# Optimization experiments

Measured on AMD Instinct MI355X. Metric: run time of the kernel, lower is better.

The kernel has to match this reference:

```python
import jax, jax.numpy as jnp
import numpy as np

NUM_HEADS = 12

def setup_inputs() -> dict:
    key = jax.random.key(0)
    k1, k2, k3, k4 = jax.random.split(key, 4)
    B, N, D = 8, 1024, 768
    x = jax.random.normal(k1, (B, N, D), dtype=jnp.float32)
    mask = jax.random.randint(k2, (B, N), 0, 2, dtype=jnp.int32)
    Wqkv = jax.random.normal(k3, (3 * D, D), dtype=jnp.float32) * (D ** -0.5)
    Wproj = jax.random.normal(k4, (D, D), dtype=jnp.float32) * (D ** -0.5)
    bproj = jnp.zeros((D,), dtype=jnp.float32)
    return {"x": x, "mask": mask, "Wqkv": Wqkv, "Wproj": Wproj, "bproj": bproj}

def reference(x, mask, Wqkv, Wproj, bproj):
    B, N, D = x.shape
    H = NUM_HEADS
    hd = D // H
    scale = hd ** -0.5
    # QKV projection (no bias), split into q,k,v of shape [B,H,N,hd]
    qkv = jnp.einsum('bnd,ed->bne', x, Wqkv).reshape(B, N, 3, H, hd)
    qkv = jnp.transpose(qkv, (2, 0, 3, 1, 4))
    q, k, v = qkv[0], qkv[1], qkv[2]
    # padding mask: attend where both query and key are valid; masked-out
    # (padded) query rows attend only to themselves (diagonal) to avoid NaNs
    m = mask.astype(bool)  # [B,N]
    pair = m[:, None, :, None] & m[:, None, None, :]          # [B,1,N,N]
    diag = jnp.eye(N, dtype=bool)[None, None]                 # [1,1,N,N]
    attn_mask = pair | (diag & ~m[:, None, :, None])          # [B,1,N,N]
    scores = jnp.einsum('bhnd,bhmd->bhnm', q, k) * scale      # [B,H,N,N]
    scores = jnp.where(attn_mask, scores, jnp.finfo(scores.dtype).min)
    attn = jax.nn.softmax(scores, axis=-1)
    out = jnp.einsum('bhnm,bhmd->bhnd', attn, v)
    out = jnp.transpose(out, (0, 2, 1, 3)).reshape(B, N, D)
    out = jnp.einsum('bnd,ed->bne', out, Wproj) + bproj
    return out
```

## Files before the change

kernel.cpp:

```cpp
#include <hip/hip_runtime.h>
#include <hip/hip_bf16.h>
#include <stdint.h>


typedef unsigned short u16;
typedef __attribute__((ext_vector_type(8))) short short8;
typedef __attribute__((ext_vector_type(4))) float f32x4;

#define MFMA16(a, b, c) __builtin_amdgcn_mfma_f32_16x16x32_bf16((a), (b), (c), 0, 0, 0)

static __device__ __forceinline__ u16 f2bf(float f) {
    __hip_bfloat16 h = __float2bfloat16(f);
    return *(u16*)&h;
}
static __device__ __forceinline__ void gld16(const u16* g, u16* l) {
  __builtin_amdgcn_global_load_lds(
      (const __attribute__((address_space(1))) void*)g,
      (__attribute__((address_space(3))) void*)l, 16, 0, 0);
}

__global__ __launch_bounds__(256) void cvt_bf16(
    const float* __restrict__ s0, u16* __restrict__ d0, int n0,
    const float* __restrict__ s1, u16* __restrict__ d1, int n1,
    const float* __restrict__ s2, u16* __restrict__ d2, int n2) {
  int i = (blockIdx.x * 256 + threadIdx.x) * 4;
  const float* s; u16* d;
  if (i < n0) { s = s0 + i; d = d0 + i; }
  else if ((i -= n0) < n1) { s = s1 + i; d = d1 + i; }
  else if ((i -= n1) < n2) { s = s2 + i; d = d2 + i; }
  else return;
  float4 v = *(const float4*)s;
  ushort4 o;
  o.x = f2bf(v.x); o.y = f2bf(v.y); o.z = f2bf(v.z); o.w = f2bf(v.w);
  *(ushort4*)d = o;
}

template<int K, int BN, int LDC, bool BF16OUT>
__global__ __launch_bounds__(256) void gemm_bt(
    const u16* __restrict__ A,
    const u16* __restrict__ B,
    void* __restrict__ Cout,
    const float* __restrict__ bias) {
  constexpr int NT = BN / 32;
  __shared__ u16 As[128 * 32];
  __shared__ u16 Bs[BN * 32];
  const int tid = threadIdx.x;
  const int w = tid >> 6, l = tid & 63;
  const int lane16 = l & 15, quad = l >> 4;
  const int i0 = blockIdx.y * 128, j0 = blockIdx.x * BN;
  const int mh = (w & 1) * 64;
  const int nh = (w >> 1) * (BN / 2);

  f32x4 acc[4][NT];
  #pragma unroll
  for (int mt = 0; mt < 4; mt++)
    #pragma unroll
    for (int nt = 0; nt < NT; nt++) acc[mt][nt] = (f32x4){0.f, 0.f, 0.f, 0.f};

  for (int kt = 0; kt < K / 32; kt++) {
    const int k0 = kt * 32;
    __syncthreads();
    #pragma unroll
    for (int s = 0; s < 2; s++) {
      int idx = tid + s * 256;
      int row = idx >> 2, c8 = (idx & 3) * 8;
      gld16(&A[(size_t)(i0 + row) * K + k0 + c8], &As[idx * 8]);
    }
    #pragma unroll
    for (int s = 0; s < BN / 64; s++) {
      int idx = tid + s * 256;
      int row = idx >> 2, c8 = (idx & 3) * 8;
      gld16(&B[(size_t)(j0 + row) * K + k0 + c8], &Bs[idx * 8]);
    }
    __syncthreads();

    short8 af[4], bf[NT];
    #pragma unroll
    for (int mt = 0; mt < 4; mt++)
      af[mt] = *(const short8*)&As[(mh + mt * 16 + lane16) * 32 + quad * 8];
    #pragma unroll
    for (int nt = 0; nt < NT; nt++)
      bf[nt] = *(const short8*)&Bs[(nh + nt * 16 + lane16) * 32 + quad * 8];
    #pragma unroll
    for (int mt = 0; mt < 4; mt++)
      #pragma unroll
      for (int nt = 0; nt < NT; nt++)
        acc[mt][nt] = MFMA16(af[mt], bf[nt], acc[mt][nt]);
  }

  #pragma unroll
  for (int mt = 0; mt < 4; mt++) {
    #pragma unroll
    for (int nt = 0; nt < NT; nt++) {
      int col = j0 + nh + nt * 16 + lane16;
      #pragma unroll
      for (int r = 0; r < 4; r++) {
        int row = i0 + mh + mt * 16 + quad * 4 + r;
        if (BF16OUT) {
          ((u16*)Cout)[(size_t)row * LDC + col] = f2bf(acc[mt][nt][r]);
        } else {
          ((float*)Cout)[(size_t)row * LDC + col] = acc[mt][nt][r] + bias[col];
        }
      }
    }
  }
}

__global__ __launch_bounds__(256, 4) void attn_mfma(
    const u16* __restrict__ qkv,
    const int* __restrict__ mask,
    u16* __restrict__ ctx) {
  __shared__ u16 Ks[64][72];
  __shared__ u16 Vt[64][72];
  __shared__ u16 Ps[4][32][72];
  __shared__ float mkb[64];
  __shared__ int mqs[128];

  const int tid = threadIdx.x;
  const int w = tid >> 6, l = tid & 63;
  const int lane16 = l & 15, quad = l >> 4;
  const int idx = blockIdx.x;
  const int bh = idx % 96;
  const int rb = idx / 96;
  const int b = bh / 12, h = bh % 12;
  const int n0 = rb * 128;
  const int baseRow = b * 1024;

  const int key_s = tid >> 2, ds_s = (tid & 3) * 16;
  const int kA_s = (tid & 31) * 2, dg_s = tid >> 5;

  if (tid < 128) mqs[tid] = mask[baseRow + n0 + tid];

  short8 qfrag[2][2];
  #pragma unroll
  for (int qt = 0; qt < 2; qt++) {
    const u16* qp = qkv + (size_t)(baseRow + n0 + w*32 + qt*16 + lane16) * 2304 + h*64;
    #pragma unroll
    for (int ks = 0; ks < 2; ks++)
      qfrag[qt][ks] = *(const short8*)(qp + ks*32 + quad*8);
  }

  f32x4 oacc[2][4];
  #pragma unroll
  for (int qt = 0; qt < 2; qt++)
    #pragma unroll
    for (int nt = 0; nt < 4; nt++) oacc[qt][nt] = (f32x4){0.f, 0.f, 0.f, 0.f};
  float lsum[2] = {0.f, 0.f};

  const float K1 = 0.18033688011112043f;
  const float K0 = -23.083120654223415f;

  for (int c = 0; c < 16; c++) {
    if (c) __syncthreads();
    {
      const u16* kp = qkv + (size_t)(baseRow + c*64 + key_s) * 2304 + 768 + h*64 + ds_s;
      uint4 kr0 = *(const uint4*)kp;
      uint4 kr1 = *(const uint4*)(kp + 8);
      const u16* vp = qkv + (size_t)(baseRow + c*64 + kA_s) * 2304 + 1536 + h*64 + dg_s*8;
      uint4 vr0 = *(const uint4*)vp;
      uint4 vr1 = *(const uint4*)(vp + 2304);
      *(uint4*)&Ks[key_s][ds_s]     = kr0;
      *(uint4*)&Ks[key_s][ds_s + 8] = kr1;
      const u16* va = (const u16*)&vr0;
      const u16* vb = (const u16*)&vr1;
      #pragma unroll
      for (int j = 0; j < 8; j++)
        *(unsigned int*)&Vt[dg_s*8 + j][kA_s] =
            (unsigned int)va[j] | ((unsigned int)vb[j] << 16);
      if (tid < 64) mkb[tid] = mask[baseRow + c*64 + tid] ? 0.f : -1e38f;
    }
    __syncthreads();

    f32x4 sacc[4][2];
    #pragma unroll
    for (int kt = 0; kt < 4; kt++)
      #pragma unroll
      for (int qt = 0; qt < 2; qt++) sacc[kt][qt] = (f32x4){0.f, 0.f, 0.f, 0.f};
    #pragma unroll
    for (int ks = 0; ks < 2; ks++) {
      short8 kf[4];
      #pragma unroll
      for (int kt = 0; kt < 4; kt++)
        kf[kt] = *(const short8*)&Ks[kt*16 + lane16][ks*32 + quad*8];
      #pragma unroll
      for (int kt = 0; kt < 4; kt++)
        #pragma unroll
        for (int qt = 0; qt < 2; qt++)
          sacc[kt][qt] = MFMA16(kf[kt], qfrag[qt][ks], sacc[kt][qt]);
    }

    #pragma unroll
    for (int kt = 0; kt < 4; kt++) {
      #pragma unroll
      for (int qt = 0; qt < 2; qt++) {
        u16 pk[4];
        #pragma unroll
        for (int r = 0; r < 4; r++) {
          int keyl = kt*16 + quad*4 + r;
          float e = __builtin_amdgcn_exp2f(fmaf(sacc[kt][qt][r], K1, K0) + mkb[keyl]);
          lsum[qt] += e;
          pk[r] = f2bf(e);
        }
        uint2 pv;
        pv.x = (unsigned int)pk[0] | ((unsigned int)pk[1] << 16);
        pv.y = (unsigned int)pk[2] | ((unsigned int)pk[3] << 16);
        *(uint2*)&Ps[w][qt*16 + lane16][kt*16 + quad*4] = pv;
      }
    }

    #pragma unroll
    for (int kc = 0; kc < 2; kc++) {
      short8 pf[2], vf[4];
      #pragma unroll
      for (int qt = 0; qt < 2; qt++)
        pf[qt] = *(const short8*)&Ps[w][qt*16 + lane16][kc*32 + quad*8];
      #pragma unroll
      for (int nt = 0; nt < 4; nt++)
        vf[nt] = *(const short8*)&Vt[nt*16 + lane16][kc*32 + quad*8];
      #pragma unroll
      for (int qt = 0; qt < 2; qt++)
        #pragma unroll
        for (int nt = 0; nt < 4; nt++)
          oacc[qt][nt] = MFMA16(pf[qt], vf[nt], oacc[qt][nt]);
    }
  }

  float linv[2][4];
  #pragma unroll
  for (int qt = 0; qt < 2; qt++) {
    float s = lsum[qt];
    s += __shfl_xor(s, 16);
    s += __shfl_xor(s, 32);
    #pragma unroll
    for (int r = 0; r < 4; r++)
      linv[qt][r] = 1.0f / __shfl(s, quad*4 + r);
  }
  #pragma unroll
  for (int qt = 0; qt < 2; qt++) {
    #pragma unroll
    for (int r = 0; r < 4; r++) {
      int rl = w*32 + qt*16 + quad*4 + r;
      int rg = n0 + rl;
      int mq = mqs[rl];
      #pragma unroll
      for (int nt = 0; nt < 4; nt++) {
        u16 outv;
        if (mq) {
          outv = f2bf(oacc[qt][nt][r] * linv[qt][r]);
        } else {
          outv = qkv[(size_t)(baseRow + rg) * 2304 + 1536 + h*64 + nt*16 + lane16];
        }
        ctx[(size_t)(baseRow + rg) * 768 + h*64 + nt*16 + lane16] = outv;
      }
    }
  }
}

extern "C" void kernel_launch(void* const* d_in, const int* in_sizes, int n_in,
                              void* d_out, int out_size, void* d_ws, size_t ws_size,
                              hipStream_t stream) {
  const float* x     = (const float*)d_in[0];
  const int*   mask  = (const int*)d_in[1];
  const float* Wqkv  = (const float*)d_in[2];
  const float* Wproj = (const float*)d_in[3];
  const float* bproj = (const float*)d_in[4];
  float* out = (float*)d_out;

  const int NX = 8192 * 768;
  const int NQ = 2304 * 768;
  const int NP = 768 * 768;

  char* wsb = (char*)d_ws;
  u16* qkv    = (u16*)wsb;
  u16* ctx    = (u16*)(wsb + (size_t)8192 * 2304 * 2);
  u16* xb     = (u16*)(wsb + (size_t)8192 * 2304 * 2 + (size_t)8192 * 768 * 2);
  u16* wqkvb  = xb + NX;
  u16* wprojb = wqkvb + NQ;

  int cvt_blocks = ((NX + NQ + NP) / 4 + 255) / 256;
  cvt_bf16<<<dim3(cvt_blocks), 256, 0, stream>>>(x, xb, NX, Wqkv, wqkvb, NQ, Wproj, wprojb, NP);

  gemm_bt<768, 128, 2304, true><<<dim3(18, 64), 256, 0, stream>>>(xb, wqkvb, qkv, nullptr);
  attn_mfma<<<dim3(768), 256, 0, stream>>>(qkv, mask, ctx);
  gemm_bt<768, 64, 768, false><<<dim3(12, 64), 256, 0, stream>>>(ctx, wprojb, out, bproj);
}
```

Measured before the change: 202.0 us.

## Prefetch next K/V chunk into registers and raise MFMA wave priority

Global loads of the next chunk's K, V and mask values are issued into registers before the current chunk's compute, then written to LDS at the top of the next iteration. This hides global-memory latency behind the MFMA and softmax work. MFMA blocks are wrapped in s_setprio to favour matrix issue, the mask bias is read as one vector load per key tile, and the row sums are split into four partial accumulators. The prefetch adds register pressure, which may lower occupancy.

```diff
diff --git a/kernel.cpp b/kernel.cpp
--- a/kernel.cpp
+++ b/kernel.cpp
@@ -145,29 +145,46 @@
   for (int qt = 0; qt < 2; qt++)
     #pragma unroll
     for (int nt = 0; nt < 4; nt++) oacc[qt][nt] = (f32x4){0.f, 0.f, 0.f, 0.f};
-  float lsum[2] = {0.f, 0.f};
+  f32x4 lsum4[2] = {(f32x4){0.f,0.f,0.f,0.f}, (f32x4){0.f,0.f,0.f,0.f}};
 
   const float K1 = 0.18033688011112043f;
   const float K0 = -23.083120654223415f;
 
+  uint4 kr0, kr1, vr0, vr1;
+  int mraw = 0;
+  {
+    const u16* kp = qkv + (size_t)(baseRow + key_s) * 2304 + 768 + h*64 + ds_s;
+    kr0 = *(const uint4*)kp;
+    kr1 = *(const uint4*)(kp + 8);
+    const u16* vp = qkv + (size_t)(baseRow + kA_s) * 2304 + 1536 + h*64 + dg_s*8;
+    vr0 = *(const uint4*)vp;
+    vr1 = *(const uint4*)(vp + 2304);
+    if (tid < 64) mraw = mask[baseRow + tid];
+  }
+
   for (int c = 0; c < 16; c++) {
     if (c) __syncthreads();
+
+    *(uint4*)&Ks[key_s][ds_s]     = kr0;
+    *(uint4*)&Ks[key_s][ds_s + 8] = kr1;
     {
-      const u16* kp = qkv + (size_t)(baseRow + c*64 + key_s) * 2304 + 768 + h*64 + ds_s;
-      uint4 kr0 = *(const uint4*)kp;
-      uint4 kr1 = *(const uint4*)(kp + 8);
-      const u16* vp = qkv + (size_t)(baseRow + c*64 + kA_s) * 2304 + 1536 + h*64 + dg_s*8;
-      uint4 vr0 = *(const uint4*)vp;
-      uint4 vr1 = *(const uint4*)(vp + 2304);
-      *(uint4*)&Ks[key_s][ds_s]     = kr0;
-      *(uint4*)&Ks[key_s][ds_s + 8] = kr1;
       const u16* va = (const u16*)&vr0;
       const u16* vb = (const u16*)&vr1;
       #pragma unroll
       for (int j = 0; j < 8; j++)
         *(unsigned int*)&Vt[dg_s*8 + j][kA_s] =
             (unsigned int)va[j] | ((unsigned int)vb[j] << 16);
-      if (tid < 64) mkb[tid] = mask[baseRow + c*64 + tid] ? 0.f : -1e38f;
+      if (tid < 64) mkb[tid] = mraw ? 0.f : -1e38f;
+    }
+
+    if (c + 1 < 16) {
+      const u16* kp = qkv + (size_t)(baseRow + (c+1)*64 + key_s) * 2304 + 768 + h*64 + ds_s;
+      kr0 = *(const uint4*)kp;
+      kr1 = *(const uint4*)(kp + 8);
+      const u16* vp = qkv + (size_t)(baseRow + (c+1)*64 + kA_s) * 2304 + 1536 + h*64 + dg_s*8;
+      vr0 = *(const uint4*)vp;
+      vr1 = *(const uint4*)(vp + 2304);
+      if (tid < 64) mraw = mask[baseRow + (c+1)*64 + tid];
     }
     __syncthreads();
 
@@ -182,23 +199,25 @@
       #pragma unroll
       for (int kt = 0; kt < 4; kt++)
         kf[kt] = *(const short8*)&Ks[kt*16 + lane16][ks*32 + quad*8];
+      __builtin_amdgcn_s_setprio(1);
       #pragma unroll
       for (int kt = 0; kt < 4; kt++)
         #pragma unroll
         for (int qt = 0; qt < 2; qt++)
           sacc[kt][qt] = MFMA16(kf[kt], qfrag[qt][ks], sacc[kt][qt]);
+      __builtin_amdgcn_s_setprio(0);
     }
 
     #pragma unroll
     for (int kt = 0; kt < 4; kt++) {
+      f32x4 mk4 = *(const f32x4*)&mkb[kt*16 + quad*4];
       #pragma unroll
       for (int qt = 0; qt < 2; qt++) {
         u16 pk[4];
         #pragma unroll
         for (int r = 0; r < 4; r++) {
-          int keyl = kt*16 + quad*4 + r;
-          float e = __builtin_amdgcn_exp2f(fmaf(sacc[kt][qt][r], K1, K0) + mkb[keyl]);
-          lsum[qt] += e;
+          float e = __builtin_amdgcn_exp2f(fmaf(sacc[kt][qt][r], K1, K0) + mk4[r]);
+          lsum4[qt][r] += e;
           pk[r] = f2bf(e);
         }
         uint2 pv;
@@ -217,18 +236,20 @@
       #pragma unroll
       for (int nt = 0; nt < 4; nt++)
         vf[nt] = *(const short8*)&Vt[nt*16 + lane16][kc*32 + quad*8];
+      __builtin_amdgcn_s_setprio(1);
       #pragma unroll
       for (int qt = 0; qt < 2; qt++)
         #pragma unroll
         for (int nt = 0; nt < 4; nt++)
           oacc[qt][nt] = MFMA16(pf[qt], vf[nt], oacc[qt][nt]);
+      __builtin_amdgcn_s_setprio(0);
     }
   }
 
   float linv[2][4];
   #pragma unroll
   for (int qt = 0; qt < 2; qt++) {
-    float s = lsum[qt];
+    float s = lsum4[qt][0] + lsum4[qt][1] + lsum4[qt][2] + lsum4[qt][3];
     s += __shfl_xor(s, 16);
     s += __shfl_xor(s, 32);
     #pragma unroll
```

After: 244.2 us. 20.9% more time.
